# Performance work log

Hardware: AMD Instinct MI355X
Metric: run time of the kernel (lower is better)

Reference implementation:

```python
import jax, jax.numpy as jnp
import numpy as np


def setup_inputs() -> dict:
    key = jax.random.key(0)
    ks = jax.random.split(key, 9)
    B, C, H, W = 16, 64, 256, 256  # N == C is required by GCN.conv1d_1
    p = lambda k, shape: jax.random.normal(k, shape, dtype=jnp.float32) * 0.05
    return {
        "x": jax.random.normal(ks[0], (B, C, H, W), dtype=jnp.float32),
        "theta_w": p(ks[1], (C, C)),   # Conv2d(C, N=C, 1) weight, squeezed to [N, C]
        "theta_b": p(ks[2], (C,)),
        "g1_w": p(ks[3], (C, C)),      # Conv1d(N, N, 1) weight, squeezed to [N, N]
        "g1_b": p(ks[4], (C,)),
        "g2_w": p(ks[5], (1, 1)),      # Conv1d(1, 1, 1) weight
        "g2_b": p(ks[6], (1,)),
        "phi_w": p(ks[7], (C,)),       # Conv2d(1, C, 1) weight, squeezed to [C]
        "phi_b": p(ks[8], (C,)),
    }


def reference(x, theta_w, theta_b, g1_w, g1_b, g2_w, g2_b, phi_w, phi_b):
    # x: [B, C, H, W], with N == C and mid_channels == 1
    # AdaptiveAvgPool2d(1): global average pool -> node features [B, C]
    x_node = jnp.mean(x, axis=(2, 3))
    # theta: 1x1 Conv2d C -> N, kept as 4D map [B, N, H, W]
    Bmap = jnp.einsum('nc,bchw->bnhw', theta_w, x) + theta_b[None, :, None, None]
    # GCN: conv1d_1 (1x1 over length-1 sequence) == dense matmul on channels
    h = x_node @ g1_w.T + g1_b                      # [B, N]
    # permute -> [B, 1, N]; conv1d_2 on the single channel is scalar affine
    z1 = h * g2_w[0, 0] + g2_b[0]                   # [B, N]
    # B^T @ z1 : contract node dim, producing the 1-channel spatial map y
    y = jnp.einsum('bnhw,bn->bhw', Bmap, z1)[:, None]  # [B, 1, H, W]
    # phi_inv: 1x1 Conv2d 1 -> C (broadcast multiply + bias)
    x_res = y * phi_w[None, :, None, None] + phi_b[None, :, None, None]
    # self.sigmoid is actually nn.Tanh()
    return jnp.tanh(x_res + x)
```

## Files before the change

### kernel.cpp

```cpp
#include <hip/hip_runtime.h>
#include <hip/hip_bf16.h>

#define B_   16
#define C_   64
#define HW_  65536
#define TILE 128

typedef float f4_t __attribute__((ext_vector_type(4)));

__device__ __forceinline__ float fast_tanh(float z) {
    z = fminf(fmaxf(z, -15.f), 15.f);
    float e = __expf(2.f * z);
    return 1.f - 2.f * __builtin_amdgcn_rcpf(e + 1.f);
}

__global__ __launch_bounds__(256) void k_reduce_mean(
    const float* __restrict__ x, float* __restrict__ x_node) {
    int bc  = blockIdx.x;
    int tid = threadIdx.x;
    const float4* p4 = (const float4*)(x + (size_t)bc * HW_);

    float s = 0.f;
#pragma unroll
    for (int i = 0; i < 64; ++i) {
        float4 v = p4[tid + 256 * i];
        s += (v.x + v.y) + (v.z + v.w);
    }
#pragma unroll
    for (int off = 32; off; off >>= 1) s += __shfl_down(s, off, 64);

    __shared__ float ls[4];
    int wid = tid >> 6, lane = tid & 63;
    if (lane == 0) ls[wid] = s;
    __syncthreads();
    if (tid == 0) {
        float t = (ls[0] + ls[1]) + (ls[2] + ls[3]);
        x_node[bc] = t * (1.0f / (float)HW_);
    }
}

__global__ __launch_bounds__(1024) void k_small(
    const float* __restrict__ x_node,
    const float* __restrict__ theta_w, const float* __restrict__ theta_b,
    const float* __restrict__ g1_w,    const float* __restrict__ g1_b,
    const float* __restrict__ g2_w,    const float* __restrict__ g2_b,
    float* __restrict__ w_eff, float* __restrict__ bias_eff) {
    int t = threadIdx.x;
    int b = t >> 6, n = t & 63;

    __shared__ float z1s[B_][C_];
    float h = g1_b[n];
#pragma unroll
    for (int c = 0; c < C_; ++c) h += x_node[b * C_ + c] * g1_w[n * C_ + c];
    float z1 = h * g2_w[0] + g2_b[0];
    z1s[b][n] = z1;
    __syncthreads();

    int c = n;
    float w = 0.f;
#pragma unroll
    for (int nn = 0; nn < C_; ++nn) w += z1s[b][nn] * theta_w[nn * C_ + c];
    w_eff[b * C_ + c] = w;

    if (c == 0) {
        float bb = 0.f;
#pragma unroll
        for (int nn = 0; nn < C_; ++nn) bb += z1s[b][nn] * theta_b[nn];
        bias_eff[b] = bb;
    }
}

__global__ __launch_bounds__(256) void k_fused_out(
    const float* __restrict__ x,
    const float* __restrict__ w_eff, const float* __restrict__ bias_eff,
    const float* __restrict__ phi_w, const float* __restrict__ phi_b,
    float* __restrict__ out) {
    __shared__ float tile[C_][TILE];
    __shared__ float ys[TILE];
    __shared__ float wsh[C_], pw[C_], pb[C_];

    int t  = threadIdx.x;
    int b  = blockIdx.x >> 9;
    int ti = blockIdx.x & 511;
    int p0 = ti * TILE;

    if (t < C_) {
        wsh[t] = w_eff[b * C_ + t];
        pw[t]  = phi_w[t];
        pb[t]  = phi_b[t];
    }

    const float* xb = x + (size_t)b * C_ * HW_ + p0;
#pragma unroll
    for (int i = 0; i < 8; ++i) {
        int f = i * 256 + t;
        int c = f >> 5;
        int j = f & 31;
        float4 v = *(const float4*)(xb + (size_t)c * HW_ + 4 * j);
        *(float4*)&tile[c][4 * j] = v;
    }
    __syncthreads();

    if (t < TILE) {
        float y = bias_eff[b];
#pragma unroll
        for (int c = 0; c < C_; ++c) y += wsh[c] * tile[c][t];
        ys[t] = y;
    }
    __syncthreads();

    float* ob = out + (size_t)b * C_ * HW_ + p0;
#pragma unroll
    for (int i = 0; i < 8; ++i) {
        int f = i * 256 + t;
        int c = f >> 5;
        int j = f & 31;
        float4 v  = *(float4*)&tile[c][4 * j];
        float4 yv = *(float4*)&ys[4 * j];
        float a = pw[c], d = pb[c];
        f4_t r;
        r.x = fast_tanh(yv.x * a + d + v.x);
        r.y = fast_tanh(yv.y * a + d + v.y);
        r.z = fast_tanh(yv.z * a + d + v.z);
        r.w = fast_tanh(yv.w * a + d + v.w);
        __builtin_nontemporal_store(r, (f4_t*)(ob + (size_t)c * HW_ + 4 * j));
    }
}

extern "C" void kernel_launch(void* const* d_in, const int* in_sizes, int n_in,
                              void* d_out, int out_size, void* d_ws, size_t ws_size,
                              hipStream_t stream) {
    const float* x       = (const float*)d_in[0];
    const float* theta_w = (const float*)d_in[1];
    const float* theta_b = (const float*)d_in[2];
    const float* g1_w    = (const float*)d_in[3];
    const float* g1_b    = (const float*)d_in[4];
    const float* g2_w    = (const float*)d_in[5];
    const float* g2_b    = (const float*)d_in[6];
    const float* phi_w   = (const float*)d_in[7];
    const float* phi_b   = (const float*)d_in[8];
    float* out = (float*)d_out;

    float* x_node   = (float*)d_ws;
    float* w_eff    = x_node + B_ * C_;
    float* bias_eff = w_eff + B_ * C_;

    k_reduce_mean<<<B_ * C_, 256, 0, stream>>>(x, x_node);
    k_small<<<1, B_ * C_, 0, stream>>>(x_node, theta_w, theta_b, g1_w, g1_b,
                                       g2_w, g2_b, w_eff, bias_eff);
    k_fused_out<<<B_ * (HW_ / TILE), 256, 0, stream>>>(x, w_eff, bias_eff,
                                                       phi_w, phi_b, out);
}
```

Before: 136.9 us.

## Process batches in cache-sized groups and fuse GCN math into reduction tail

Splits the batch into groups of four and runs the mean reduction and the fused output pass per group. The aim is for the second read of x to hit the large last-level cache instead of HBM. The small GCN/weight-folding kernel is merged into the last finishing reduction block per batch, using an atomic counter and thread fences. Each channel is also split across two blocks for more parallelism. This adds more kernel launches, a memset, and atomic-based cross-block synchronization.

```diff
diff --git a/kernel.cpp b/kernel.cpp
--- a/kernel.cpp
+++ b/kernel.cpp
@@ -5,6 +5,8 @@
 #define C_   64
 #define HW_  65536
 #define TILE 128
+#define GB   4
+#define NG   (B_ / GB)
 
 typedef float f4_t __attribute__((ext_vector_type(4)));
 
@@ -14,64 +16,85 @@
     return 1.f - 2.f * __builtin_amdgcn_rcpf(e + 1.f);
 }
 
-__global__ __launch_bounds__(256) void k_reduce_mean(
-    const float* __restrict__ x, float* __restrict__ x_node) {
-    int bc  = blockIdx.x;
-    int tid = threadIdx.x;
-    const float4* p4 = (const float4*)(x + (size_t)bc * HW_);
+__global__ __launch_bounds__(256) void k_reduce_group(
+    const float* __restrict__ x, int b0,
+    const float* __restrict__ theta_w, const float* __restrict__ theta_b,
+    const float* __restrict__ g1_w,    const float* __restrict__ g1_b,
+    const float* __restrict__ g2_w,    const float* __restrict__ g2_b,
+    float* __restrict__ part, float* __restrict__ w_eff,
+    float* __restrict__ bias_eff, int* __restrict__ cnt) {
+    int t    = threadIdx.x;
+    int blk  = blockIdx.x;
+    int half = blk & 1;
+    int bcl  = blk >> 1;
+    int b    = b0 + (bcl >> 6);
+    int c    = bcl & 63;
+    int bc   = b * C_ + c;
 
+    const float4* p4 = (const float4*)(x + (size_t)bc * HW_ + half * (HW_ / 2));
     float s = 0.f;
 #pragma unroll
-    for (int i = 0; i < 64; ++i) {
-        float4 v = p4[tid + 256 * i];
+    for (int i = 0; i < 32; ++i) {
+        float4 v = p4[t + 256 * i];
         s += (v.x + v.y) + (v.z + v.w);
     }
 #pragma unroll
     for (int off = 32; off; off >>= 1) s += __shfl_down(s, off, 64);
 
     __shared__ float ls[4];
-    int wid = tid >> 6, lane = tid & 63;
+    __shared__ int amlast;
+    int wid = t >> 6, lane = t & 63;
     if (lane == 0) ls[wid] = s;
     __syncthreads();
-    if (tid == 0) {
-        float t = (ls[0] + ls[1]) + (ls[2] + ls[3]);
-        x_node[bc] = t * (1.0f / (float)HW_);
+    if (t == 0) {
+        part[bc * 2 + half] = (ls[0] + ls[1]) + (ls[2] + ls[3]);
+        __threadfence();
+        int old = atomicAdd(&cnt[b], 1);
+        amlast = (old == 2 * C_ - 1);
     }
-}
+    __syncthreads();
+    if (!amlast) return;
 
-__global__ __launch_bounds__(1024) void k_small(
-    const float* __restrict__ x_node,
-    const float* __restrict__ theta_w, const float* __restrict__ theta_b,
-    const float* __restrict__ g1_w,    const float* __restrict__ g1_b,
-    const float* __restrict__ g2_w,    const float* __restrict__ g2_b,
-    float* __restrict__ w_eff, float* __restrict__ bias_eff) {
-    int t = threadIdx.x;
-    int b = t >> 6, n = t & 63;
-
-    __shared__ float z1s[B_][C_];
-    float h = g1_b[n];
+    __threadfence();
+    __shared__ float xn[C_], z1s[C_], hp[4][C_], wp[4][C_];
+    int n = t & 63, q = t >> 6;
+    if (t < C_) {
+        float p0 = part[(b * C_ + t) * 2], p1 = part[(b * C_ + t) * 2 + 1];
+        xn[t] = (p0 + p1) * (1.0f / (float)HW_);
+    }
+    __syncthreads();
+    float hpart = 0.f;
 #pragma unroll
-    for (int c = 0; c < C_; ++c) h += x_node[b * C_ + c] * g1_w[n * C_ + c];
-    float z1 = h * g2_w[0] + g2_b[0];
-    z1s[b][n] = z1;
+    for (int i = 0; i < 16; ++i) {
+        int cc = q * 16 + i;
+        hpart += xn[cc] * g1_w[n * C_ + cc];
+    }
+    hp[q][n] = hpart;
     __syncthreads();
-
-    int c = n;
-    float w = 0.f;
+    if (t < C_) {
+        float h = g1_b[t] + (hp[0][t] + hp[1][t]) + (hp[2][t] + hp[3][t]);
+        z1s[t] = h * g2_w[0] + g2_b[0];
+    }
+    __syncthreads();
+    float wpart = 0.f;
 #pragma unroll
-    for (int nn = 0; nn < C_; ++nn) w += z1s[b][nn] * theta_w[nn * C_ + c];
-    w_eff[b * C_ + c] = w;
-
-    if (c == 0) {
+    for (int i = 0; i < 16; ++i) {
+        int nn = q * 16 + i;
+        wpart += z1s[nn] * theta_w[nn * C_ + n];
+    }
+    wp[q][n] = wpart;
+    __syncthreads();
+    if (t < C_) w_eff[b * C_ + t] = (wp[0][t] + wp[1][t]) + (wp[2][t] + wp[3][t]);
+    if (t == 0) {
         float bb = 0.f;
 #pragma unroll
-        for (int nn = 0; nn < C_; ++nn) bb += z1s[b][nn] * theta_b[nn];
+        for (int nn = 0; nn < C_; ++nn) bb += z1s[nn] * theta_b[nn];
         bias_eff[b] = bb;
     }
 }
 
 __global__ __launch_bounds__(256) void k_fused_out(
-    const float* __restrict__ x,
+    const float* __restrict__ x, int b0,
     const float* __restrict__ w_eff, const float* __restrict__ bias_eff,
     const float* __restrict__ phi_w, const float* __restrict__ phi_b,
     float* __restrict__ out) {
@@ -80,7 +103,7 @@
     __shared__ float wsh[C_], pw[C_], pb[C_];
 
     int t  = threadIdx.x;
-    int b  = blockIdx.x >> 9;
+    int b  = b0 + (blockIdx.x >> 9);
     int ti = blockIdx.x & 511;
     int p0 = ti * TILE;
 
@@ -141,13 +164,19 @@
     const float* phi_b   = (const float*)d_in[8];
     float* out = (float*)d_out;
 
-    float* x_node   = (float*)d_ws;
-    float* w_eff    = x_node + B_ * C_;
+    float* part     = (float*)d_ws;
+    float* w_eff    = part + B_ * C_ * 2;
     float* bias_eff = w_eff + B_ * C_;
+    int*   cnt      = (int*)(bias_eff + B_);
 
-    k_reduce_mean<<<B_ * C_, 256, 0, stream>>>(x, x_node);
-    k_small<<<1, B_ * C_, 0, stream>>>(x_node, theta_w, theta_b, g1_w, g1_b,
-                                       g2_w, g2_b, w_eff, bias_eff);
-    k_fused_out<<<B_ * (HW_ / TILE), 256, 0, stream>>>(x, w_eff, bias_eff,
-                                                       phi_w, phi_b, out);
+    hipMemsetAsync(cnt, 0, B_ * sizeof(int), stream);
+
+    for (int g = 0; g < NG; ++g) {
+        int b0 = g * GB;
+        k_reduce_group<<<GB * C_ * 2, 256, 0, stream>>>(
+            x, b0, theta_w, theta_b, g1_w, g1_b, g2_w, g2_b,
+            part, w_eff, bias_eff, cnt);
+        k_fused_out<<<GB * (HW_ / TILE), 256, 0, stream>>>(
+            x, b0, w_eff, bias_eff, phi_w, phi_b, out);
+    }
 }
```

After: 207.2 us. 1.51x slower.
